# Kernel optimization log

Hardware: AMD Instinct MI355X
Metric: run time of the kernel (lower is better)

## Reference

```python
import jax, jax.numpy as jnp
import numpy as np

EPS = 1e-07
INF = 100000.0
BIG = 1e8  # sentinel cost for priors outside all gt boxes/centers (filtered out in torch)
CENTER_RADIUS = 2.5
CANDIDATE_TOPK = 10
IOU_WEIGHT = 3.0
CLS_WEIGHT = 1.0
IMG = 1280.0


def setup_inputs() -> dict:
    key = jax.random.key(0)
    ks = jax.random.split(key, 9)
    N, G, C = 33600, 128, 80
    cx = jax.random.uniform(ks[0], (N,), minval=0.0, maxval=IMG)
    cy = jax.random.uniform(ks[1], (N,), minval=0.0, maxval=IMG)
    strides = jax.random.uniform(ks[2], (N, 2), minval=8.0, maxval=32.0)
    priors = jnp.stack([cx, cy, strides[:, 0], strides[:, 1]], axis=1)  # [N,4] cx,cy,sw,sh
    dc = jax.random.uniform(ks[3], (N, 2), minval=0.0, maxval=IMG)
    dwh = jax.random.uniform(ks[4], (N, 2), minval=4.0, maxval=200.0)
    decoded_bboxes = jnp.concatenate([dc - dwh / 2, dc + dwh / 2], axis=1)  # [N,4] tlbr
    gc = jax.random.uniform(ks[5], (G, 2), minval=0.0, maxval=IMG)
    gwh = jax.random.uniform(ks[6], (G, 2), minval=20.0, maxval=400.0)
    gt_bboxes = jnp.concatenate([gc - gwh / 2, gc + gwh / 2], axis=1)  # [G,4] tlbr
    pred_scores = jax.random.uniform(ks[7], (N, C), minval=1e-4, maxval=1.0 - 1e-4)
    gt_labels = jax.random.randint(ks[8], (G,), 0, C)
    return {
        'pred_scores': pred_scores,
        'priors': priors,
        'decoded_bboxes': decoded_bboxes,
        'gt_bboxes': gt_bboxes,
        'gt_labels': gt_labels,
    }


def _pairwise_iou(a, b):
    # a: [N,4] tlbr, b: [G,4] tlbr -> [N,G]
    tl = jnp.maximum(a[:, None, :2], b[None, :, :2])
    br = jnp.minimum(a[:, None, 2:], b[None, :, 2:])
    wh = jnp.clip(br - tl, 0.0)
    inter = wh[..., 0] * wh[..., 1]
    area_a = jnp.prod(jnp.clip(a[:, 2:] - a[:, :2], 0.0), axis=-1)
    area_b = jnp.prod(jnp.clip(b[:, 2:] - b[:, :2], 0.0), axis=-1)
    union = area_a[:, None] + area_b[None, :] - inter
    return inter / jnp.maximum(union, EPS)


def _forward(pred_scores, priors, decoded_bboxes, gt_bboxes, gt_labels):
    N = decoded_bboxes.shape[0]
    G = gt_bboxes.shape[0]
    px, py = priors[:, 0:1], priors[:, 1:2]          # [N,1]
    sx, sy = priors[:, 2:3], priors[:, 3:4]
    # in-gt-box mask [N,G]
    l_ = px - gt_bboxes[None, :, 0]
    t_ = py - gt_bboxes[None, :, 1]
    r_ = gt_bboxes[None, :, 2] - px
    b_ = gt_bboxes[None, :, 3] - py
    is_in_gts = jnp.minimum(jnp.minimum(l_, t_), jnp.minimum(r_, b_)) > 0
    # in-center mask [N,G]
    gcx = (gt_bboxes[:, 0] + gt_bboxes[:, 2]) / 2.0
    gcy = (gt_bboxes[:, 1] + gt_bboxes[:, 3]) / 2.0
    cl_ = px - (gcx[None, :] - CENTER_RADIUS * sx)
    ct_ = py - (gcy[None, :] - CENTER_RADIUS * sy)
    cr_ = (gcx[None, :] + CENTER_RADIUS * sx) - px
    cb_ = (gcy[None, :] + CENTER_RADIUS * sy) - py
    is_in_cts = jnp.minimum(jnp.minimum(cl_, ct_), jnp.minimum(cr_, cb_)) > 0
    valid = jnp.any(is_in_gts | is_in_cts, axis=1)           # [N]
    in_box_and_center = is_in_gts & is_in_cts                # [N,G]

    ious = _pairwise_iou(decoded_bboxes, gt_bboxes)          # [N,G]
    ious = jnp.where(valid[:, None], ious, 0.0)              # invalid priors excluded
    iou_cost = -jnp.log(ious + EPS)

    # BCE(pred, one_hot(label)).sum(-1) without materializing [N,G,C]:
    # = -log p[label] + log1p(-p[label]) - sum_c log1p(-p_c)  (logs clamped at -100 like torch)
    L = jnp.clip(jnp.log(pred_scores), -100.0)               # [N,C]
    L1 = jnp.clip(jnp.log1p(-pred_scores), -100.0)           # [N,C]
    gl = gt_labels.astype(jnp.int32)
    cls_cost = -(L[:, gl] - L1[:, gl]) - jnp.sum(L1, axis=1, keepdims=True)  # [N,G]

    cost = cls_cost * CLS_WEIGHT + iou_cost * IOU_WEIGHT + (~in_box_and_center) * INF
    cost = jnp.where(valid[:, None], cost, BIG)

    K = min(CANDIDATE_TOPK, N)
    topk_ious, _ = jax.lax.top_k(ious.T, K)                  # [G,K]
    dynamic_ks = jnp.clip(topk_ious.sum(1).astype(jnp.int32), 1, None)  # [G], <= K
    # per-GT: K smallest costs (ascending), keep first dynamic_k of them
    _, pos_idx = jax.lax.top_k(-cost.T, K)                   # [G,K] prior indices
    sel = (jnp.arange(K)[None, :] < dynamic_ks[:, None]).astype(cost.dtype)
    matching = jnp.zeros((N, G), cost.dtype).at[pos_idx, jnp.arange(G)[:, None]].add(sel)

    # resolve priors matched to >1 gt by min-cost gt
    multi = matching.sum(1) > 1
    argmin = jnp.argmin(cost, axis=1)
    matching = jnp.where(multi[:, None], jax.nn.one_hot(argmin, G, dtype=cost.dtype), matching)

    fg = matching.sum(1) > 0
    matched_gt = jnp.argmax(matching, axis=1)
    matched_iou = jnp.sum(matching * ious, axis=1)

    assigned_gt_inds = jnp.where(fg, matched_gt, 0)
    assigned_labels = jnp.where(fg, 1, -1)
    assigned_gt_iou = jnp.where(fg, matched_iou, -INF)
    return assigned_gt_inds, assigned_labels, assigned_gt_iou


def reference(pred_scores, priors, decoded_bboxes, gt_bboxes, gt_labels):
    return _forward(pred_scores, priors, decoded_bboxes, gt_bboxes, gt_labels)
```

## Files before the change

### kernel.cpp

```cpp
#include <hip/hip_runtime.h>
#include <math.h>
#include <limits.h>

#pragma clang fp contract(off)

#define TPB 256
#define ATPB 64
#define KTOP 10
#define ISPLIT 64
#define GSPLIT 8
#define GSLICE 4352
#define MAXG 512

typedef unsigned int u32;
typedef unsigned long long u64;
typedef unsigned char u8;

__device__ __forceinline__ float f_iou(float ax0, float ay0, float ax1, float ay1,
                                       float bx0, float by0, float bx1, float by1) {
  float tlx = fmaxf(ax0, bx0);
  float tly = fmaxf(ay0, by0);
  float brx = fminf(ax1, bx1);
  float bry = fminf(ay1, by1);
  float w = fmaxf(brx - tlx, 0.0f);
  float h = fmaxf(bry - tly, 0.0f);
  float inter = w * h;
  float aa = fmaxf(ax1 - ax0, 0.0f) * fmaxf(ay1 - ay0, 0.0f);
  float ab = fmaxf(bx1 - bx0, 0.0f) * fmaxf(by1 - by0, 0.0f);
  float uni = aa + ab - inter;
  return inter / fmaxf(uni, 1e-7f);
}

__device__ __forceinline__ float f_dv(float p) {
  float L  = fmaxf(logf(p), -100.0f);
  float L1 = fmaxf(log1pf(-p), -100.0f);
  return -(L - L1);
}

__device__ __forceinline__ float f_cost(float iou_masked, float dv, float sumL1v,
                                        float px, float py, float sx, float sy,
                                        float bx0, float by0, float bx1, float by1,
                                        int vld) {
  if (!vld) return 100000000.0f;
  float cls = dv - sumL1v;
  float l_ = px - bx0, t_ = py - by0, r_ = bx1 - px, b_ = by1 - py;
  bool ing = fminf(fminf(l_, t_), fminf(r_, b_)) > 0.0f;
  float gcx = (bx0 + bx1) * 0.5f;
  float gcy = (by0 + by1) * 0.5f;
  float cl = px - (gcx - 2.5f * sx);
  float ct = py - (gcy - 2.5f * sy);
  float cr = (gcx + 2.5f * sx) - px;
  float cb = (gcy + 2.5f * sy) - py;
  bool inc = fminf(fminf(cl, ct), fminf(cr, cb)) > 0.0f;
  float icost = -logf(iou_masked + 1e-7f);
  return (cls * 1.0f + icost * 3.0f) + ((ing && inc) ? 0.0f : 100000.0f);
}

__global__ __launch_bounds__(TPB) void k_fb(float* out, int Nout, float val) {
  int n = blockIdx.x * blockDim.x + threadIdx.x;
  if (n >= Nout) return;
  out[n] = 0.0f;
  out[Nout + n] = -1.0f;
  out[2 * Nout + n] = val;
}

__global__ __launch_bounds__(TPB) void k_phase1(
    const float* pred, const float* priors, const float* gtb,
    float* sumL1, u32* packed, u8* validArr,
    int* gateCnt2, int* gateList,
    int N, int G, int C, int sumBlocks)
{
  __shared__ float sg[MAXG * 4];
  __shared__ int lbuf[GSLICE];
  __shared__ int lcnt;
  const int tid = threadIdx.x;
  const int lane = tid & 63;
  const float4* pri4 = reinterpret_cast<const float4*>(priors);

  if ((int)blockIdx.x < sumBlocks) {
    for (int i = tid; i < G * 4; i += TPB) sg[i] = gtb[i];
    __syncthreads();
    int t = blockIdx.x * TPB + tid;
    int n = t >> 3, j = t & 7;
    if (n >= N) return;
    float4 pv = pri4[n];
    float px = pv.x, py = pv.y, sx = pv.z, sy = pv.w;
    int valid = 0;
    for (int g = j; g < G; g += 8) {
      float x0 = sg[g * 4 + 0], y0 = sg[g * 4 + 1], x1 = sg[g * 4 + 2], y1 = sg[g * 4 + 3];
      float l_ = px - x0, t_ = py - y0, r_ = x1 - px, b_ = y1 - py;
      bool ing = fminf(fminf(l_, t_), fminf(r_, b_)) > 0.0f;
      float gcx = (x0 + x1) * 0.5f, gcy = (y0 + y1) * 0.5f;
      float cl = px - (gcx - 2.5f * sx), ct = py - (gcy - 2.5f * sy);
      float cr = (gcx + 2.5f * sx) - px, cb = (gcy + 2.5f * sy) - py;
      bool inc = fminf(fminf(cl, ct), fminf(cr, cb)) > 0.0f;
      valid |= (ing || inc) ? 1 : 0;
    }
    valid |= __shfl_xor(valid, 1, 8);
    valid |= __shfl_xor(valid, 2, 8);
    valid |= __shfl_xor(valid, 4, 8);
    const float* pr = pred + (size_t)n * C;
    int lim = C - (C % 8);
    float r = 0.0f;
    for (int i = j; i < lim; i += 8) r += fmaxf(log1pf(-pr[i]), -100.0f);
    r += __shfl_down(r, 1, 8);
    r += __shfl_down(r, 2, 8);
    r += __shfl_down(r, 4, 8);
    if (j == 0) {
      for (int i = lim; i < C; ++i) r += fmaxf(log1pf(-pr[i]), -100.0f);
      sumL1[n] = r;
      validArr[n] = (u8)valid;
      packed[n] = 0;
    }
    return;
  }

  int bidg = blockIdx.x - sumBlocks;
  int g = bidg / GSPLIT, s = bidg % GSPLIT;
  int chunk = (N + GSPLIT - 1) / GSPLIT;
  int start = s * chunk;
  int end = start + chunk; if (end > N) end = N;
  float x0 = gtb[g * 4 + 0], y0 = gtb[g * 4 + 1];
  float x1 = gtb[g * 4 + 2], y1 = gtb[g * 4 + 3];
  float gcx = (x0 + x1) * 0.5f, gcy = (y0 + y1) * 0.5f;
  if (tid == 0) lcnt = 0;
  __syncthreads();
  for (int nb = start; nb < end; nb += TPB) {
    int n = nb + tid;
    bool gated = false;
    if (n < end) {
      float4 pv = pri4[n];
      float px = pv.x, py = pv.y, sx = pv.z, sy = pv.w;
      float l_ = px - x0, t_ = py - y0, r_ = x1 - px, b_ = y1 - py;
      bool ing = fminf(fminf(l_, t_), fminf(r_, b_)) > 0.0f;
      float cl = px - (gcx - 2.5f * sx), ct = py - (gcy - 2.5f * sy);
      float cr = (gcx + 2.5f * sx) - px, cb = (gcy + 2.5f * sy) - py;
      bool inc = fminf(fminf(cl, ct), fminf(cr, cb)) > 0.0f;
      gated = ing && inc;
    }
    u64 mask = __ballot(gated);
    int wcnt = __popcll(mask);
    int wbase = 0;
    if (lane == 0 && wcnt > 0) wbase = atomicAdd(&lcnt, wcnt);
    wbase = __shfl(wbase, 0);
    if (gated) {
      int p = __popcll(mask & ((1ull << lane) - 1ull));
      lbuf[wbase + p] = n;
    }
  }
  __syncthreads();
  int total = lcnt;
  if (tid == 0) gateCnt2[bidg] = total;
  int* gl = gateList + (size_t)bidg * GSLICE;
  for (int i = tid; i < total; i += TPB) gl[i] = lbuf[i];
}

__global__ __launch_bounds__(ATPB) void k_iou_part(
    const float* dec, const u8* validArr, const float* gtb,
    float* iouV, int N, int G)
{
  int bid = blockIdx.x;
  int g = bid / ISPLIT;
  int s = bid % ISPLIT;
  int chunk = (N + ISPLIT - 1) / ISPLIT;
  int start = s * chunk;
  int end = start + chunk; if (end > N) end = N;
  int tid = threadIdx.x;
  float bx0 = gtb[g * 4 + 0];
  float by0 = gtb[g * 4 + 1];
  float bx1 = gtb[g * 4 + 2];
  float by1 = gtb[g * 4 + 3];

  float iv[KTOP];
#pragma unroll
  for (int j = 0; j < KTOP; ++j) iv[j] = 0.0f;

  const float4* dec4 = reinterpret_cast<const float4*>(dec);
  for (int n = start + tid; n < end; n += ATPB) {
    float4 dvb = dec4[n];
    float iou = f_iou(dvb.x, dvb.y, dvb.z, dvb.w, bx0, by0, bx1, by1);
    if (!validArr[n]) iou = 0.0f;
    if (iou > iv[KTOP - 1]) {
      float cu = iou;
#pragma unroll
      for (int j = 0; j < KTOP; ++j) {
        if (cu > iv[j]) { float tv = iv[j]; iv[j] = cu; cu = tv; }
      }
    }
  }

#pragma unroll
  for (int r = 0; r < KTOP; ++r) {
    float v = iv[0]; int owner = tid;
#pragma unroll
    for (int off = 32; off > 0; off >>= 1) {
      float v2 = __shfl_down(v, off);
      int o2 = __shfl_down(owner, off);
      if (v2 > v || (v2 == v && o2 < owner)) { v = v2; owner = o2; }
    }
    float wv = __shfl(v, 0);
    int wo = __shfl(owner, 0);
    if (tid == 0) iouV[bid * KTOP + r] = wv;
    if (tid == wo) {
#pragma unroll
      for (int j = 0; j < KTOP - 1; ++j) iv[j] = iv[j + 1];
      iv[KTOP - 1] = 0.0f;
    }
  }
}

__global__ __launch_bounds__(ATPB) void k_merge(
    const float* iouV, const int* gateCnt2, const int* gateList,
    const float* pred, const float* priors, const float* dec, const float* sumL1,
    const u8* validArr, const int* gtl, const float* gtb,
    u32* packed, int G, int N, int C)
{
  int g = blockIdx.x;
  int tid = threadIdx.x;
  int base = g * ISPLIT * KTOP;
  const int TOT = ISPLIT * KTOP;
  const int PER = TOT / ATPB;

  float il[PER];
#pragma unroll
  for (int k = 0; k < PER; ++k) il[k] = 0.0f;
#pragma unroll
  for (int k = 0; k < PER; ++k) {
    float v = iouV[base + tid + k * ATPB];
    if (v > il[PER - 1]) {
#pragma unroll
      for (int j = 0; j < PER; ++j) {
        if (v > il[j]) { float tv = il[j]; il[j] = v; v = tv; }
      }
    }
  }
  float rv[KTOP];
#pragma unroll
  for (int r = 0; r < KTOP; ++r) {
    float v = il[0]; int owner = tid;
#pragma unroll
    for (int off = 32; off > 0; off >>= 1) {
      float v2 = __shfl_down(v, off);
      int o2 = __shfl_down(owner, off);
      if (v2 > v || (v2 == v && o2 < owner)) { v = v2; owner = o2; }
    }
    float wv = __shfl(v, 0);
    int wo = __shfl(owner, 0);
    rv[r] = wv;
    if (tid == wo) {
#pragma unroll
      for (int j = 0; j < PER - 1; ++j) il[j] = il[j + 1];
      il[PER - 1] = 0.0f;
    }
  }
  float s8 = ((rv[0] + rv[1]) + (rv[2] + rv[3])) + ((rv[4] + rv[5]) + (rv[6] + rv[7]));
  s8 += rv[8];
  s8 += rv[9];
  int dk = (int)s8;
  if (dk < 1) dk = 1;
  if (dk > KTOP) dk = KTOP;

  float bx0 = gtb[g * 4 + 0], by0 = gtb[g * 4 + 1];
  float bx1 = gtb[g * 4 + 2], by1 = gtb[g * 4 + 3];
  int lab = gtl[g];
  if (lab < 0) lab = 0;
  if (lab >= C) lab = C - 1;

  float cv[KTOP]; int ci[KTOP];
#pragma unroll
  for (int j = 0; j < KTOP; ++j) { cv[j] = 1e30f; ci[j] = INT_MAX; }
  const float4* dec4 = reinterpret_cast<const float4*>(dec);

  int total = 0;
  for (int s = 0; s < GSPLIT; ++s) total += gateCnt2[g * GSPLIT + s];

  if (total >= KTOP) {
    for (int s = 0; s < GSPLIT; ++s) {
      int cs = gateCnt2[g * GSPLIT + s];
      const int* gl = gateList + (size_t)(g * GSPLIT + s) * GSLICE;
      for (int i = tid; i < cs; i += ATPB) {
        int n = gl[i];
        float4 d = dec4[n];
        float iou = f_iou(d.x, d.y, d.z, d.w, bx0, by0, bx1, by1);
        float dv = f_dv(pred[(size_t)n * C + lab]);
        float cls = dv - sumL1[n];
        float icost = -logf(iou + 1e-7f);
        float c = (cls * 1.0f + icost * 3.0f) + 0.0f;
        bool ins = (c < cv[KTOP - 1]) || (c == cv[KTOP - 1] && n < ci[KTOP - 1]);
        if (ins) {
          float cu = c; int cui = n;
#pragma unroll
          for (int j = 0; j < KTOP; ++j) {
            bool lt = (cu < cv[j]) || (cu == cv[j] && cui < ci[j]);
            if (lt) { float tv = cv[j]; int ti = ci[j]; cv[j] = cu; ci[j] = cui; cu = tv; cui = ti; }
          }
        }
      }
    }
  } else {
    const float4* pri4 = reinterpret_cast<const float4*>(priors);
    for (int n = tid; n < N; n += ATPB) {
      float4 d = dec4[n];
      int vld = validArr[n];
      float iou = f_iou(d.x, d.y, d.z, d.w, bx0, by0, bx1, by1);
      if (!vld) iou = 0.0f;
      float dv = f_dv(pred[(size_t)n * C + lab]);
      float4 pv = pri4[n];
      float c = f_cost(iou, dv, sumL1[n], pv.x, pv.y, pv.z, pv.w,
                       bx0, by0, bx1, by1, vld);
      bool ins = (c < cv[KTOP - 1]) || (c == cv[KTOP - 1] && n < ci[KTOP - 1]);
      if (ins) {
        float cu = c; int cui = n;
#pragma unroll
        for (int j = 0; j < KTOP; ++j) {
          bool lt = (cu < cv[j]) || (cu == cv[j] && cui < ci[j]);
          if (lt) { float tv = cv[j]; int ti = ci[j]; cv[j] = cu; ci[j] = cui; cu = tv; cui = ti; }
        }
      }
    }
  }

  for (int r = 0; r < KTOP; ++r) {
    float v = cv[0]; int idx = ci[0];
#pragma unroll
    for (int off = 32; off > 0; off >>= 1) {
      float v2 = __shfl_down(v, off);
      int i2 = __shfl_down(idx, off);
      if (v2 < v || (v2 == v && i2 < idx)) { v = v2; idx = i2; }
    }
    int wi = __shfl(idx, 0);
    if (r < dk && tid == 0 && wi >= 0 && wi < N) {
      atomicAdd(&packed[wi], (1u << 16) | (u32)g);
    }
    if (ci[0] == wi && wi != INT_MAX) {
#pragma unroll
      for (int j = 0; j < KTOP - 1; ++j) { cv[j] = cv[j + 1]; ci[j] = ci[j + 1]; }
      cv[KTOP - 1] = 1e30f; ci[KTOP - 1] = INT_MAX;
    }
    if (r + 1 >= dk) break;
  }
}

__global__ __launch_bounds__(TPB) void k_phase3(
    const float* pred, const float* priors, const float* dec,
    const float* gtb, const int* gtl, const float* sumL1,
    const u8* validArr, const u32* packed,
    float* out, int N, int G, int C, int Nout)
{
  __shared__ float sg[MAXG * 4];
  __shared__ int sl[MAXG];
  for (int i = threadIdx.x; i < G * 4; i += blockDim.x) sg[i] = gtb[i];
  for (int i = threadIdx.x; i < G; i += blockDim.x) {
    int lb = gtl[i];
    if (lb < 0) lb = 0;
    if (lb >= C) lb = C - 1;
    sl[i] = lb;
  }
  __syncthreads();
  const int tid = threadIdx.x;
  const int lane = tid & 63;
  const float4* dec4 = reinterpret_cast<const float4*>(dec);
  const float4* pri4 = reinterpret_cast<const float4*>(priors);
  int n = blockIdx.x * TPB + tid;
  bool active = (n < N && n < Nout);
  u32 pk = active ? packed[n] : 0;
  int cnt = (int)(pk >> 16);

  if (active && cnt <= 1) {
    float o0 = 0.0f, o1 = -1.0f, o2 = -100000.0f;
    if (cnt == 1) {
      int g = (int)(pk & 0xFFFFu);
      if (g < 0) g = 0;
      if (g >= G) g = G - 1;
      float4 d = dec4[n];
      float x0 = sg[g * 4 + 0], y0 = sg[g * 4 + 1], x1 = sg[g * 4 + 2], y1 = sg[g * 4 + 3];
      float iou = f_iou(d.x, d.y, d.z, d.w, x0, y0, x1, y1);
      if (!validArr[n]) iou = 0.0f;
      o0 = (float)g; o1 = 1.0f; o2 = iou;
    }
    out[n]            = o0;
    out[Nout + n]     = o1;
    out[2 * Nout + n] = o2;
  }

  u64 mm = __ballot(active && cnt > 1);
  while (mm) {
    int l = (int)(__ffsll((unsigned long long)mm) - 1);
    mm &= mm - 1;
    int mn = __shfl(n, l);
    float4 dvb = dec4[mn];
    float4 pv = pri4[mn];
    float s1 = sumL1[mn];
    int vld = validArr[mn];
    float best = 1e30f; int bg = INT_MAX;
    for (int gg = lane; gg < G; gg += 64) {
      float x0 = sg[gg * 4 + 0], y0 = sg[gg * 4 + 1];
      float x1 = sg[gg * 4 + 2], y1 = sg[gg * 4 + 3];
      float iou = f_iou(dvb.x, dvb.y, dvb.z, dvb.w, x0, y0, x1, y1);
      if (!vld) iou = 0.0f;
      float dv = f_dv(pred[(size_t)mn * C + sl[gg]]);
      float c = f_cost(iou, dv, s1, pv.x, pv.y, pv.z, pv.w, x0, y0, x1, y1, vld);
      if (c < best || (c == best && gg < bg)) { best = c; bg = gg; }
    }
#pragma unroll
    for (int off = 32; off > 0; off >>= 1) {
      float v2 = __shfl_down(best, off);
      int g2 = __shfl_down(bg, off);
      if (v2 < best || (v2 == best && g2 < bg)) { best = v2; bg = g2; }
    }
    int wg = __shfl(bg, 0);
    if (lane == 0) {
      int g = (wg < 0 || wg >= G) ? 0 : wg;
      float x0 = sg[g * 4 + 0], y0 = sg[g * 4 + 1];
      float x1 = sg[g * 4 + 2], y1 = sg[g * 4 + 3];
      float iou = f_iou(dvb.x, dvb.y, dvb.z, dvb.w, x0, y0, x1, y1);
      if (!vld) iou = 0.0f;
      out[mn]            = (float)g;
      out[Nout + mn]     = 1.0f;
      out[2 * Nout + mn] = iou;
    }
  }
}

extern "C" void kernel_launch(void* const* d_in, const int* in_sizes, int n_in,
                              void* d_out, int out_size, void* d_ws, size_t ws_size,
                              hipStream_t stream) {
  const float* pred   = (const float*)d_in[0];
  const float* priors = (const float*)d_in[1];
  const float* dec    = (const float*)d_in[2];
  const float* gtb    = (const float*)d_in[3];
  const int*   gtl    = (const int*)d_in[4];
  int N = in_sizes[2] / 4;
  int G = in_sizes[3] / 4;
  int C = in_sizes[0] / N;
  int Nout = out_size / 3;
  float* out = (float*)d_out;

  dim3 b(TPB);
  int oblk = (Nout + TPB - 1) / TPB;
  int chunk = (N + GSPLIT - 1) / GSPLIT;
  if (G > MAXG || chunk > GSLICE) {
    k_fb<<<oblk, b, 0, stream>>>(out, Nout, -60000.0f);
    return;
  }

  size_t offPacked = 0;
  size_t offSum    = offPacked + (size_t)N * 4;
  size_t offValid  = offSum + (size_t)N * 4;
  size_t offCnt2   = (offValid + (size_t)N + 15) & ~(size_t)15;
  size_t offGlist  = (offCnt2 + (size_t)G * GSPLIT * 4 + 15) & ~(size_t)15;
  size_t offIouV   = offGlist + (size_t)G * GSPLIT * GSLICE * 4;
  size_t need      = offIouV + (size_t)G * ISPLIT * KTOP * 4;
  if (ws_size < need || d_ws == nullptr) {
    k_fb<<<oblk, b, 0, stream>>>(out, Nout, -70000.0f);
    return;
  }
  char* wsb = (char*)d_ws;
  u32* packed   = (u32*)(wsb + offPacked);
  float* sumL1  = (float*)(wsb + offSum);
  u8* validArr  = (u8*)(wsb + offValid);
  int* gateCnt2 = (int*)(wsb + offCnt2);
  int* gateList = (int*)(wsb + offGlist);
  float* iouV   = (float*)(wsb + offIouV);

  int sumBlocks = (N * 8 + TPB - 1) / TPB;
  int nblk = (N + TPB - 1) / TPB;
  k_phase1<<<sumBlocks + G * GSPLIT, b, 0, stream>>>(
      pred, priors, gtb, sumL1, packed, validArr, gateCnt2, gateList,
      N, G, C, sumBlocks);
  k_iou_part<<<G * ISPLIT, dim3(ATPB), 0, stream>>>(dec, validArr, gtb, iouV, N, G);
  k_merge<<<G, dim3(ATPB), 0, stream>>>(
      iouV, gateCnt2, gateList, pred, priors, dec, sumL1, validArr, gtl, gtb,
      packed, G, N, C);
  k_phase3<<<nblk, b, 0, stream>>>(
      pred, priors, dec, gtb, gtl, sumL1, validArr, packed,
      out, N, G, C, Nout);
}
```

Baseline: 135.0 us.

## Move class-sum into IoU kernel and flatten merge gate-list loop

Moves the per-prior log1p class-sum computation out of the first kernel and into the IoU top-k kernel, so the memory-heavy pred scan runs concurrently with the IoU partial top-k instead of before it. The IoU kernel now packs four 64-lane units per 256-thread block. The merge kernel replaces the nested per-slice loop over gate lists with one flat loop over a shared prefix sum, balancing threads across slices. The cost is a per-element slice search and an extra block-level sync.

```diff
diff --git a/kernel.cpp b/kernel.cpp
--- a/kernel.cpp
+++ b/kernel.cpp
@@ -64,20 +64,17 @@
   out[2 * Nout + n] = val;
 }
 
-__global__ __launch_bounds__(TPB) void k_phase1(
-    const float* pred, const float* priors, const float* gtb,
-    float* sumL1, u32* packed, u8* validArr,
-    int* gateCnt2, int* gateList,
-    int N, int G, int C, int sumBlocks)
+__global__ __launch_bounds__(TPB) void k_prep(
+    const float* priors, const float* gtb,
+    u8* validArr, int* gateCnt2, int* gateList,
+    int N, int G, int valBlocks)
 {
-  __shared__ float sg[MAXG * 4];
-  __shared__ int lbuf[GSLICE];
-  __shared__ int lcnt;
   const int tid = threadIdx.x;
   const int lane = tid & 63;
   const float4* pri4 = reinterpret_cast<const float4*>(priors);
 
-  if ((int)blockIdx.x < sumBlocks) {
+  if ((int)blockIdx.x < valBlocks) {
+    __shared__ float sg[MAXG * 4];
     for (int i = tid; i < G * 4; i += TPB) sg[i] = gtb[i];
     __syncthreads();
     int t = blockIdx.x * TPB + tid;
@@ -99,23 +96,13 @@
     valid |= __shfl_xor(valid, 1, 8);
     valid |= __shfl_xor(valid, 2, 8);
     valid |= __shfl_xor(valid, 4, 8);
-    const float* pr = pred + (size_t)n * C;
-    int lim = C - (C % 8);
-    float r = 0.0f;
-    for (int i = j; i < lim; i += 8) r += fmaxf(log1pf(-pr[i]), -100.0f);
-    r += __shfl_down(r, 1, 8);
-    r += __shfl_down(r, 2, 8);
-    r += __shfl_down(r, 4, 8);
-    if (j == 0) {
-      for (int i = lim; i < C; ++i) r += fmaxf(log1pf(-pr[i]), -100.0f);
-      sumL1[n] = r;
-      validArr[n] = (u8)valid;
-      packed[n] = 0;
-    }
+    if (j == 0) validArr[n] = (u8)valid;
     return;
   }
 
-  int bidg = blockIdx.x - sumBlocks;
+  __shared__ int lbuf[GSLICE];
+  __shared__ int lcnt;
+  int bidg = blockIdx.x - valBlocks;
   int g = bidg / GSPLIT, s = bidg % GSPLIT;
   int chunk = (N + GSPLIT - 1) / GSPLIT;
   int start = s * chunk;
@@ -155,28 +142,49 @@
   for (int i = tid; i < total; i += TPB) gl[i] = lbuf[i];
 }
 
-__global__ __launch_bounds__(ATPB) void k_iou_part(
-    const float* dec, const u8* validArr, const float* gtb,
-    float* iouV, int N, int G)
+__global__ __launch_bounds__(TPB) void k_sumiou(
+    const float* pred, const float* dec, const u8* validArr, const float* gtb,
+    float* sumL1, u32* packed, float* iouV,
+    int N, int G, int C, int sumBlocks)
 {
-  int bid = blockIdx.x;
-  int g = bid / ISPLIT;
-  int s = bid % ISPLIT;
+  const int tid = threadIdx.x;
+  const int lane = tid & 63;
+  const int wid = tid >> 6;
+
+  if ((int)blockIdx.x < sumBlocks) {
+    int t = blockIdx.x * TPB + tid;
+    int n = t >> 3, j = t & 7;
+    if (n >= N) return;
+    const float* pr = pred + (size_t)n * C;
+    int lim = C - (C % 8);
+    float r = 0.0f;
+    for (int i = j; i < lim; i += 8) r += fmaxf(log1pf(-pr[i]), -100.0f);
+    r += __shfl_down(r, 1, 8);
+    r += __shfl_down(r, 2, 8);
+    r += __shfl_down(r, 4, 8);
+    if (j == 0) {
+      for (int i = lim; i < C; ++i) r += fmaxf(log1pf(-pr[i]), -100.0f);
+      sumL1[n] = r;
+      packed[n] = 0;
+    }
+    return;
+  }
+
+  int unit = ((int)blockIdx.x - sumBlocks) * 4 + wid;
+  if (unit >= G * ISPLIT) return;
+  int g = unit / ISPLIT, s = unit % ISPLIT;
   int chunk = (N + ISPLIT - 1) / ISPLIT;
   int start = s * chunk;
   int end = start + chunk; if (end > N) end = N;
-  int tid = threadIdx.x;
-  float bx0 = gtb[g * 4 + 0];
-  float by0 = gtb[g * 4 + 1];
-  float bx1 = gtb[g * 4 + 2];
-  float by1 = gtb[g * 4 + 3];
+  float bx0 = gtb[g * 4 + 0], by0 = gtb[g * 4 + 1];
+  float bx1 = gtb[g * 4 + 2], by1 = gtb[g * 4 + 3];
 
   float iv[KTOP];
 #pragma unroll
   for (int j = 0; j < KTOP; ++j) iv[j] = 0.0f;
 
   const float4* dec4 = reinterpret_cast<const float4*>(dec);
-  for (int n = start + tid; n < end; n += ATPB) {
+  for (int n = start + lane; n < end; n += 64) {
     float4 dvb = dec4[n];
     float iou = f_iou(dvb.x, dvb.y, dvb.z, dvb.w, bx0, by0, bx1, by1);
     if (!validArr[n]) iou = 0.0f;
@@ -191,7 +199,7 @@
 
 #pragma unroll
   for (int r = 0; r < KTOP; ++r) {
-    float v = iv[0]; int owner = tid;
+    float v = iv[0]; int owner = lane;
 #pragma unroll
     for (int off = 32; off > 0; off >>= 1) {
       float v2 = __shfl_down(v, off);
@@ -200,8 +208,8 @@
     }
     float wv = __shfl(v, 0);
     int wo = __shfl(owner, 0);
-    if (tid == 0) iouV[bid * KTOP + r] = wv;
-    if (tid == wo) {
+    if (lane == 0) iouV[unit * KTOP + r] = wv;
+    if (lane == wo) {
 #pragma unroll
       for (int j = 0; j < KTOP - 1; ++j) iv[j] = iv[j + 1];
       iv[KTOP - 1] = 0.0f;
@@ -220,6 +228,13 @@
   int base = g * ISPLIT * KTOP;
   const int TOT = ISPLIT * KTOP;
   const int PER = TOT / ATPB;
+  __shared__ int scum[GSPLIT + 1];
+
+  if (tid == 0) {
+    int t = 0;
+    scum[0] = 0;
+    for (int s = 0; s < GSPLIT; ++s) { t += gateCnt2[g * GSPLIT + s]; scum[s + 1] = t; }
+  }
 
   float il[PER];
 #pragma unroll
@@ -271,29 +286,28 @@
   for (int j = 0; j < KTOP; ++j) { cv[j] = 1e30f; ci[j] = INT_MAX; }
   const float4* dec4 = reinterpret_cast<const float4*>(dec);
 
-  int total = 0;
-  for (int s = 0; s < GSPLIT; ++s) total += gateCnt2[g * GSPLIT + s];
+  __syncthreads();
+  int total = scum[GSPLIT];
 
   if (total >= KTOP) {
-    for (int s = 0; s < GSPLIT; ++s) {
-      int cs = gateCnt2[g * GSPLIT + s];
-      const int* gl = gateList + (size_t)(g * GSPLIT + s) * GSLICE;
-      for (int i = tid; i < cs; i += ATPB) {
-        int n = gl[i];
-        float4 d = dec4[n];
-        float iou = f_iou(d.x, d.y, d.z, d.w, bx0, by0, bx1, by1);
-        float dv = f_dv(pred[(size_t)n * C + lab]);
-        float cls = dv - sumL1[n];
-        float icost = -logf(iou + 1e-7f);
-        float c = (cls * 1.0f + icost * 3.0f) + 0.0f;
-        bool ins = (c < cv[KTOP - 1]) || (c == cv[KTOP - 1] && n < ci[KTOP - 1]);
-        if (ins) {
-          float cu = c; int cui = n;
-#pragma unroll
-          for (int j = 0; j < KTOP; ++j) {
-            bool lt = (cu < cv[j]) || (cu == cv[j] && cui < ci[j]);
-            if (lt) { float tv = cv[j]; int ti = ci[j]; cv[j] = cu; ci[j] = cui; cu = tv; cui = ti; }
-          }
+    for (int i = tid; i < total; i += ATPB) {
+      int s = 0;
+      while (i >= scum[s + 1]) ++s;
+      int idx = i - scum[s];
+      int n = gateList[(size_t)(g * GSPLIT + s) * GSLICE + idx];
+      float4 d = dec4[n];
+      float iou = f_iou(d.x, d.y, d.z, d.w, bx0, by0, bx1, by1);
+      float dv = f_dv(pred[(size_t)n * C + lab]);
+      float cls = dv - sumL1[n];
+      float icost = -logf(iou + 1e-7f);
+      float c = (cls * 1.0f + icost * 3.0f) + 0.0f;
+      bool ins = (c < cv[KTOP - 1]) || (c == cv[KTOP - 1] && n < ci[KTOP - 1]);
+      if (ins) {
+        float cu = c; int cui = n;
+#pragma unroll
+        for (int j = 0; j < KTOP; ++j) {
+          bool lt = (cu < cv[j]) || (cu == cv[j] && cui < ci[j]);
+          if (lt) { float tv = cv[j]; int ti = ci[j]; cv[j] = cu; ci[j] = cui; cu = tv; cui = ti; }
         }
       }
     }
@@ -463,12 +477,15 @@
   int* gateList = (int*)(wsb + offGlist);
   float* iouV   = (float*)(wsb + offIouV);
 
+  int valBlocks = (N * 8 + TPB - 1) / TPB;
   int sumBlocks = (N * 8 + TPB - 1) / TPB;
+  int iouBlocks = (G * ISPLIT + 3) / 4;
   int nblk = (N + TPB - 1) / TPB;
-  k_phase1<<<sumBlocks + G * GSPLIT, b, 0, stream>>>(
-      pred, priors, gtb, sumL1, packed, validArr, gateCnt2, gateList,
-      N, G, C, sumBlocks);
-  k_iou_part<<<G * ISPLIT, dim3(ATPB), 0, stream>>>(dec, validArr, gtb, iouV, N, G);
+
+  k_prep<<<valBlocks + G * GSPLIT, b, 0, stream>>>(
+      priors, gtb, validArr, gateCnt2, gateList, N, G, valBlocks);
+  k_sumiou<<<sumBlocks + iouBlocks, b, 0, stream>>>(
+      pred, dec, validArr, gtb, sumL1, packed, iouV, N, G, C, sumBlocks);
   k_merge<<<G, dim3(ATPB), 0, stream>>>(
       iouV, gateCnt2, gateList, pred, priors, dec, sumL1, validArr, gtl, gtb,
       packed, G, N, C);
```

New measurement: 129.2 us. -4.3%, faster.
